# Optimization experiments

Measured on AMD Instinct MI355X. Metric: run time of the kernel, lower is better.

The kernel has to match this reference:

```python
import jax, jax.numpy as jnp
import numpy as np
from jax import lax

N_FFT = 512
HOP = 128
Q = N_FFT // HOP  # 4
KW = 2 * N_FFT - 1  # conv kernel width 1023


def _hann_periodic(n: int) -> np.ndarray:
    # scipy.signal.get_window('hann', n) default fftbins=True -> periodic hann
    k = np.arange(n)
    return (0.5 - 0.5 * np.cos(2.0 * np.pi * k / n)).astype(np.float64)


def _compute_alpha(W: np.ndarray, S: np.ndarray) -> np.ndarray:
    # Faithful port of ConsistencyLoss._compute_alpha (paper eq. 9)
    N, R = N_FFT, HOP
    alpha = np.zeros((2 * Q - 1, 2 * N - 1), dtype=np.complex64)
    for qi, q in enumerate(range(-(Q - 1), Q)):
        S_sh = np.zeros(N)
        s0, s1 = max(0, -q * R), min(N, N - q * R)
        if s0 < s1:
            S_sh[s0:s1] = S[q * R + s0: q * R + s1]
        term = W * S_sh
        f = np.fft.fft(term, 2 * N - 1)
        alpha[qi] = np.fft.fftshift(f) / N
    alpha[Q - 1, N - 1] -= 1.0
    return alpha


def setup_inputs() -> dict:
    key = jax.random.key(0)
    waveform = 0.1 * jax.random.normal(key, (4, 131072), dtype=jnp.float32)
    W_np = _hann_periodic(N_FFT)
    alpha = _compute_alpha(W_np, W_np)
    return {
        "waveform": waveform,
        "window": jnp.asarray(W_np, dtype=jnp.float32),
        "alpha_real": jnp.asarray(alpha.real, dtype=jnp.float32),
        "alpha_imag": jnp.asarray(alpha.imag, dtype=jnp.float32),
    }


def _stft(waveform, window):
    # torch.stft(center=True, pad_mode='reflect', onesided=True), output (B, T, F)
    N, hop = N_FFT, HOP
    B, L = waveform.shape
    padded = jnp.pad(waveform, ((0, 0), (N // 2, N // 2)), mode="reflect")
    T = 1 + L // hop
    idx = hop * jnp.arange(T)[:, None] + jnp.arange(N)[None, :]  # (T, N)
    frames = padded[:, idx] * window  # (B, T, N)
    return jnp.fft.rfft(frames, axis=-1)  # (B, T, N//2+1) complex64


def reference(waveform, window, alpha_real, alpha_imag):
    N, hop = N_FFT, HOP
    B = waveform.shape[0]
    H = _stft(waveform, window)  # (B, T, N//2+1)
    T = H.shape[1]

    # reconstruct full two-sided spectrum: concat conj-flipped interior bins
    H_full = jnp.concatenate([H, jnp.conj(H[:, :, 1:-1][:, :, ::-1])], axis=2)  # (B, T, N)
    H_full = jnp.transpose(H_full, (0, 2, 1))  # (B, N, T)

    # fuse the phase-term einsum into the per-frequency conv kernel:
    # C[b,n,t] = sum_q phase[n,q] * (alpha[q] * H_full[b,n])(t)
    #          = (K_eff[n] * H_full[b,n])(t),  K_eff = phase @ alpha
    q_idx = jnp.arange(-(Q - 1), Q, dtype=jnp.float32)
    n_idx = jnp.arange(N, dtype=jnp.float32)
    phase = jnp.exp(1j * (2.0 * jnp.pi / N) * n_idx[:, None] * q_idx[None, :])  # (N, 2Q-1)
    alpha = alpha_real + 1j * alpha_imag  # (2Q-1, KW)
    K = phase @ alpha.astype(jnp.complex64)  # (N, KW)
    Kr, Ki = jnp.real(K), jnp.imag(K)

    # complex depthwise (groups=N) cross-correlation via real 2-channel trick
    Hri = jnp.stack([jnp.real(H_full), jnp.imag(H_full)], axis=2).reshape(B, 2 * N, T)
    kern = jnp.stack([
        jnp.stack([Kr, -Ki], axis=1),  # real output rows (N, 2, KW)
        jnp.stack([Ki, Kr], axis=1),   # imag output rows (N, 2, KW)
    ], axis=1).reshape(2 * N, 2, KW)
    out = lax.conv_general_dilated(
        Hri, kern, window_strides=(1,), padding=[(N - 1, N - 1)],
        dimension_numbers=("NCH", "OIH", "NCH"), feature_group_count=N,
    )  # (B, 2N, T)
    Cr, Ci = out[:, 0::2], out[:, 1::2]  # (B, N, T)

    loss = jnp.sum(Cr * Cr + Ci * Ci)
    return loss / (B * T)
```

## Files before the change

### kernel.cpp

```cpp
#include <hip/hip_runtime.h>
#include <math.h>

#define T_FRAMES 1025
#define TSTRIDE  1032
#define BATCH    4
#define LWAV     131072
#define KWC      1023
#define MFFT     2048
#define PI_F     3.14159265358979323846f

struct c32 { float r, i; };
__device__ __forceinline__ c32 mkc(float r, float i){ c32 z; z.r=r; z.i=i; return z; }
__device__ __forceinline__ c32 cadd(c32 a, c32 b){ return mkc(a.r+b.r, a.i+b.i); }
__device__ __forceinline__ c32 csub(c32 a, c32 b){ return mkc(a.r-b.r, a.i-b.i); }
__device__ __forceinline__ c32 cmul(c32 a, c32 b){ return mkc(a.r*b.r - a.i*b.i, a.r*b.i + a.i*b.r); }
__device__ __forceinline__ c32 cni(c32 a){ return mkc(a.i, -a.r); }
#define C8F 0.70710678118654752440f
__device__ __forceinline__ c32 c8p(c32 a){ return mkc(C8F*(a.r+a.i), C8F*(a.i-a.r)); }
__device__ __forceinline__ c32 c8m(c32 a){ return mkc(C8F*(a.i-a.r), -C8F*(a.r+a.i)); }

__device__ __forceinline__ void st2(float2* X, int p, c32 v){ X[p] = make_float2(v.r, v.i); }
__device__ __forceinline__ c32 ld2(const float2* X, int p){ float2 e = X[p]; return mkc(e.x, e.y); }

__device__ __forceinline__ int pX(int j){ return j + (j >> 5); }
__device__ __forceinline__ int pS2(int j){ return j + (j >> 4); }
__device__ __forceinline__ int rev9(int j){ return (int)(__brev((unsigned)j) >> 23); }

__device__ __forceinline__ c32 wexp(int r) {
    float s, c;
    __sincosf((float)r * (-PI_F / 1024.0f), &s, &c);
    return mkc(c, s);
}

__device__ __forceinline__ void dif8_tw(c32 y[8], c32 w3) {
    c32 w2 = cmul(w3, w3), w1 = cmul(w2, w2);
    c32 u[8], v[8], d;
    d = csub(y[0], y[4]); u[0] = cadd(y[0], y[4]); u[4] = cmul(d, w3);
    d = csub(y[1], y[5]); u[1] = cadd(y[1], y[5]); u[5] = c8p(cmul(d, w3));
    d = csub(y[2], y[6]); u[2] = cadd(y[2], y[6]); u[6] = cni(cmul(d, w3));
    d = csub(y[3], y[7]); u[3] = cadd(y[3], y[7]); u[7] = c8m(cmul(d, w3));
    d = csub(u[0], u[2]); v[0] = cadd(u[0], u[2]); v[2] = cmul(d, w2);
    d = csub(u[1], u[3]); v[1] = cadd(u[1], u[3]); v[3] = cni(cmul(d, w2));
    d = csub(u[4], u[6]); v[4] = cadd(u[4], u[6]); v[6] = cmul(d, w2);
    d = csub(u[5], u[7]); v[5] = cadd(u[5], u[7]); v[7] = cni(cmul(d, w2));
    d = csub(v[0], v[1]); y[0] = cadd(v[0], v[1]); y[1] = cmul(d, w1);
    d = csub(v[2], v[3]); y[2] = cadd(v[2], v[3]); y[3] = cmul(d, w1);
    d = csub(v[4], v[5]); y[4] = cadd(v[4], v[5]); y[5] = cmul(d, w1);
    d = csub(v[6], v[7]); y[6] = cadd(v[6], v[7]); y[7] = cmul(d, w1);
}
__device__ __forceinline__ void dif8_nt(c32 y[8]) {
    c32 u[8], v[8], d;
    d = csub(y[0], y[4]); u[0] = cadd(y[0], y[4]); u[4] = d;
    d = csub(y[1], y[5]); u[1] = cadd(y[1], y[5]); u[5] = c8p(d);
    d = csub(y[2], y[6]); u[2] = cadd(y[2], y[6]); u[6] = cni(d);
    d = csub(y[3], y[7]); u[3] = cadd(y[3], y[7]); u[7] = c8m(d);
    d = csub(u[0], u[2]); v[0] = cadd(u[0], u[2]); v[2] = d;
    d = csub(u[1], u[3]); v[1] = cadd(u[1], u[3]); v[3] = cni(d);
    d = csub(u[4], u[6]); v[4] = cadd(u[4], u[6]); v[6] = d;
    d = csub(u[5], u[7]); v[5] = cadd(u[5], u[7]); v[7] = cni(d);
    d = csub(v[0], v[1]); y[0] = cadd(v[0], v[1]); y[1] = d;
    d = csub(v[2], v[3]); y[2] = cadd(v[2], v[3]); y[3] = d;
    d = csub(v[4], v[5]); y[4] = cadd(v[4], v[5]); y[5] = d;
    d = csub(v[6], v[7]); y[6] = cadd(v[6], v[7]); y[7] = d;
}
__device__ __forceinline__ void dit8_tw(c32 y[8], c32 w3) {
    c32 w2 = cmul(w3, w3), w1 = cmul(w2, w2);
    c32 u[8], v[8], t;
    t = cmul(y[1], w1); u[0] = cadd(y[0], t); u[1] = csub(y[0], t);
    t = cmul(y[3], w1); u[2] = cadd(y[2], t); u[3] = csub(y[2], t);
    t = cmul(y[5], w1); u[4] = cadd(y[4], t); u[5] = csub(y[4], t);
    t = cmul(y[7], w1); u[6] = cadd(y[6], t); u[7] = csub(y[6], t);
    t = cmul(u[2], w2);      v[0] = cadd(u[0], t); v[2] = csub(u[0], t);
    t = cni(cmul(u[3], w2)); v[1] = cadd(u[1], t); v[3] = csub(u[1], t);
    t = cmul(u[6], w2);      v[4] = cadd(u[4], t); v[6] = csub(u[4], t);
    t = cni(cmul(u[7], w2)); v[5] = cadd(u[5], t); v[7] = csub(u[5], t);
    t = cmul(v[4], w3);      y[0] = cadd(v[0], t); y[4] = csub(v[0], t);
    t = c8p(cmul(v[5], w3)); y[1] = cadd(v[1], t); y[5] = csub(v[1], t);
    t = cni(cmul(v[6], w3)); y[2] = cadd(v[2], t); y[6] = csub(v[2], t);
    t = c8m(cmul(v[7], w3)); y[3] = cadd(v[3], t); y[7] = csub(v[3], t);
}
__device__ __forceinline__ void dit8_nt(c32 y[8]) {
    c32 u[8], v[8], t;
    u[0] = cadd(y[0], y[1]); u[1] = csub(y[0], y[1]);
    u[2] = cadd(y[2], y[3]); u[3] = csub(y[2], y[3]);
    u[4] = cadd(y[4], y[5]); u[5] = csub(y[4], y[5]);
    u[6] = cadd(y[6], y[7]); u[7] = csub(y[6], y[7]);
    t = u[2];      v[0] = cadd(u[0], t); v[2] = csub(u[0], t);
    t = cni(u[3]); v[1] = cadd(u[1], t); v[3] = csub(u[1], t);
    t = u[6];      v[4] = cadd(u[4], t); v[6] = csub(u[4], t);
    t = cni(u[7]); v[5] = cadd(u[5], t); v[7] = csub(u[5], t);
    t = v[4];      y[0] = cadd(v[0], t); y[4] = csub(v[0], t);
    t = c8p(v[5]); y[1] = cadd(v[1], t); y[5] = csub(v[1], t);
    t = cni(v[6]); y[2] = cadd(v[2], t); y[6] = csub(v[2], t);
    t = c8m(v[7]); y[3] = cadd(v[3], t); y[7] = csub(v[3], t);
}
__device__ __forceinline__ void dif4(c32 y[4]) {
    c32 u0 = cadd(y[0], y[2]), d0 = csub(y[0], y[2]);
    c32 u1 = cadd(y[1], y[3]), d1 = cni(csub(y[1], y[3]));
    y[0] = cadd(u0, u1); y[1] = csub(u0, u1);
    y[2] = cadd(d0, d1); y[3] = csub(d0, d1);
}
__device__ __forceinline__ void dit4(c32 y[4], c32 w) {
    c32 w2 = cmul(w, w);
    c32 t1 = cmul(y[1], w2); c32 u0 = cadd(y[0], t1), u1 = csub(y[0], t1);
    c32 t3 = cmul(y[3], w2); c32 u2 = cadd(y[2], t3), u3 = csub(y[2], t3);
    c32 s2 = cmul(u2, w);      y[0] = cadd(u0, s2); y[2] = csub(u0, s2);
    c32 s3 = cni(cmul(u3, w)); y[1] = cadd(u1, s3); y[3] = csub(u1, s3);
}

__global__ __launch_bounds__(256) void stage1_kernel(const float* __restrict__ wave,
                                                     const float* __restrict__ win,
                                                     const float* __restrict__ ar,
                                                     const float* __restrict__ ai,
                                                     float2* __restrict__ Ht,
                                                     float2* __restrict__ Afbr,
                                                     float* __restrict__ out) {
    __shared__ float2 S2[4352];
    const int tid = threadIdx.x;

    if (blockIdx.x < 516) {
        float2* F = S2;
        const int w = tid >> 6, l = tid & 63;
        const int b = blockIdx.x / 129;
        const int t0 = (blockIdx.x - b * 129) << 3;
        const float* wb = wave + (size_t)b * LWAV;

        for (int pass = 0; pass < 2; ++pass) {
            const int j = w + (pass << 2);
            const int t = t0 + j;
            if (t < T_FRAMES) {
                c32 y[8];
#pragma unroll
                for (int k = 0; k < 8; ++k) {
                    int s = l + (k << 6);
                    int posn = t * 128 + s - 256;
                    int ix = posn < 0 ? -posn : (posn >= LWAV ? 2 * LWAV - 2 - posn : posn);
                    y[k] = mkc(wb[ix] * win[s], 0.f);
                }
                dif8_tw(y, wexp(l << 2));
#pragma unroll
                for (int k = 0; k < 8; ++k) st2(F, j*544 + pS2(l + (k << 6)), y[k]);
                __builtin_amdgcn_wave_barrier();
                {
                    int base = ((l >> 3) << 6) + (l & 7);
#pragma unroll
                    for (int k = 0; k < 8; ++k) y[k] = ld2(F, j*544 + pS2(base + (k << 3)));
                    dif8_tw(y, wexp((l & 7) << 5));
#pragma unroll
                    for (int k = 0; k < 8; ++k) st2(F, j*544 + pS2(base + (k << 3)), y[k]);
                }
                __builtin_amdgcn_wave_barrier();
                {
#pragma unroll
                    for (int k = 0; k < 8; ++k) y[k] = ld2(F, j*544 + pS2((l << 3) + k));
                    dif8_nt(y);
#pragma unroll
                    for (int k = 0; k < 8; ++k) st2(F, j*544 + pS2((l << 3) + k), y[k]);
                }
            }
        }
        __syncthreads();
        const bool full = (t0 + 7 < T_FRAMES);
#pragma unroll
        for (int h = 0; h < 2; ++h) {
            int p = tid + (h << 8);
            int bin = rev9(p);
            if (bin > 256) continue;
            int ps = pS2(p);
            size_t rowbase = (size_t)(b * 512 + p) * TSTRIDE + t0;
            if (full) {
                float4* dst = (float4*)(Ht + rowbase);
#pragma unroll
                for (int jj = 0; jj < 4; ++jj) {
                    float2 e0 = F[(2*jj)*544 + ps], e1 = F[(2*jj+1)*544 + ps];
                    dst[jj] = make_float4(e0.x, e0.y, e1.x, e1.y);
                }
            } else {
                for (int jj = 0; jj < 8; ++jj)
                    if (t0 + jj < T_FRAMES) Ht[rowbase + jj] = F[jj*544 + ps];
            }
        }
    } else if (blockIdx.x < 523) {
        float2* X = S2;
        const int q = blockIdx.x - 516;
        c32 y[8];
#pragma unroll
        for (int k = 0; k < 8; ++k) {
            int j = tid + (k << 8);
            y[k] = (j < KWC) ? mkc(ar[q * KWC + j], -ai[q * KWC + j]) : mkc(0.f, 0.f);
        }
        dif8_tw(y, wexp(tid));
#pragma unroll
        for (int k = 0; k < 8; ++k) st2(X, pX(tid + (k << 8)), y[k]);
        __syncthreads();
        {
            int base = ((tid >> 5) << 8) + (tid & 31);
#pragma unroll
            for (int k = 0; k < 8; ++k) y[k] = ld2(X, pX(base + (k << 5)));
            dif8_tw(y, wexp((tid & 31) << 3));
#pragma unroll
            for (int k = 0; k < 8; ++k) st2(X, pX(base + (k << 5)), y[k]);
        }
        __syncthreads();
        {
            int base = ((tid & 63) << 5) + (tid >> 6);
#pragma unroll
            for (int k = 0; k < 8; ++k) y[k] = ld2(X, pX(base + (k << 2)));
            dif8_tw(y, wexp((tid >> 6) << 6));
#pragma unroll
            for (int k = 0; k < 8; ++k) st2(X, pX(base + (k << 2)), y[k]);
        }
        __syncthreads();
#pragma unroll
        for (int h = 0; h < 2; ++h) {
            int g = tid + (h << 8);
            c32 z4[4];
#pragma unroll
            for (int k = 0; k < 4; ++k) z4[k] = ld2(X, pX((g << 2) + k));
            dif4(z4);
#pragma unroll
            for (int k = 0; k < 4; ++k) Afbr[(q << 11) + (g << 2) + k] = make_float2(z4[k].r, -z4[k].i);
        }
    } else {
        if (tid == 0) *out = 0.f;
    }
}

__global__ __launch_bounds__(256) void conv_kernel(const float2* __restrict__ Ht,
                                                   const float2* __restrict__ Afbr,
                                                   float* __restrict__ out) {
    __shared__ float2 S2[4224];
    __shared__ float red[4];
    float2* X0 = S2;
    float2* X1 = S2 + 2112;
    const int tid = threadIdx.x;
    const int g = blockIdx.x;
    const int half = g / 257;
    const int n = g - half * 257;
    const int b0 = half << 1;
    const int pr = rev9(n);

    const float2* row0 = Ht + (size_t)(b0 * 512 + pr) * TSTRIDE;
    const float2* row1 = Ht + (size_t)((b0 + 1) * 512 + pr) * TSTRIDE;

    c32 y0[8], y1[8];
#pragma unroll
    for (int k = 0; k < 8; ++k) {
        int j = tid + (k << 8);
        c32 v0 = mkc(0.f, 0.f), v1 = mkc(0.f, 0.f);
        if (j < T_FRAMES) {
            float2 h0 = row0[j]; v0 = mkc(h0.x, h0.y);
            float2 h1 = row1[j]; v1 = mkc(h1.x, h1.y);
        }
        y0[k] = v0; y1[k] = v1;
    }
    {
        c32 w3 = wexp(tid);
        dif8_tw(y0, w3);
        dif8_tw(y1, w3);
#pragma unroll
        for (int k = 0; k < 8; ++k) {
            int p = pX(tid + (k << 8));
            st2(X0, p, y0[k]); st2(X1, p, y1[k]);
        }
    }
    __syncthreads();
    {
        int base = ((tid >> 5) << 8) + (tid & 31);
#pragma unroll
        for (int k = 0; k < 8; ++k) {
            int p = pX(base + (k << 5));
            y0[k] = ld2(X0, p); y1[k] = ld2(X1, p);
        }
        c32 w3 = wexp((tid & 31) << 3);
        dif8_tw(y0, w3);
        dif8_tw(y1, w3);
#pragma unroll
        for (int k = 0; k < 8; ++k) {
            int p = pX(base + (k << 5));
            st2(X0, p, y0[k]); st2(X1, p, y1[k]);
        }
    }
    __syncthreads();
    {
        int base = ((tid & 63) << 5) + (tid >> 6);
#pragma unroll
        for (int k = 0; k < 8; ++k) {
            int p = pX(base + (k << 2));
            y0[k] = ld2(X0, p); y1[k] = ld2(X1, p);
        }
        c32 w3 = wexp((tid >> 6) << 6);
        dif8_tw(y0, w3);
        dif8_tw(y1, w3);
#pragma unroll
        for (int k = 0; k < 8; ++k) {
            int p = pX(base + (k << 2));
            st2(X0, p, y0[k]); st2(X1, p, y1[k]);
        }
    }
    __syncthreads();
    {
        c32 p1 = wexp(-(n << 2));
        c32 p2 = cmul(p1, p1);
        c32 p3 = cmul(p2, p1);
        const int a0 = tid << 3;
        const int p0 = pX(a0);
#pragma unroll
        for (int k = 0; k < 8; ++k) {
            y0[k] = ld2(X0, p0 + k);
            y1[k] = ld2(X1, p0 + k);
        }
        dif4(&y0[0]); dif4(&y0[4]);
        dif4(&y1[0]); dif4(&y1[4]);
        const float4* af4 = (const float4*)(Afbr + a0);
#pragma unroll
        for (int k = 0; k < 8; ++k) {
            float4 a;
            c32 Kk;
            a = af4[(3 << 10) + (k >> 1)];
            float ax = (k & 1) ? a.z : a.x, ay = (k & 1) ? a.w : a.y;
            Kk = mkc(ax, ay);
            a = af4[(4 << 10) + (k >> 1)]; ax = (k & 1) ? a.z : a.x; ay = (k & 1) ? a.w : a.y;
            Kk.r += p1.r * ax - p1.i * ay;  Kk.i += p1.r * ay + p1.i * ax;
            a = af4[(2 << 10) + (k >> 1)]; ax = (k & 1) ? a.z : a.x; ay = (k & 1) ? a.w : a.y;
            Kk.r += p1.r * ax + p1.i * ay;  Kk.i += p1.r * ay - p1.i * ax;
            a = af4[(5 << 10) + (k >> 1)]; ax = (k & 1) ? a.z : a.x; ay = (k & 1) ? a.w : a.y;
            Kk.r += p2.r * ax - p2.i * ay;  Kk.i += p2.r * ay + p2.i * ax;
            a = af4[(1 << 10) + (k >> 1)]; ax = (k & 1) ? a.z : a.x; ay = (k & 1) ? a.w : a.y;
            Kk.r += p2.r * ax + p2.i * ay;  Kk.i += p2.r * ay - p2.i * ax;
            a = af4[(6 << 10) + (k >> 1)]; ax = (k & 1) ? a.z : a.x; ay = (k & 1) ? a.w : a.y;
            Kk.r += p3.r * ax - p3.i * ay;  Kk.i += p3.r * ay + p3.i * ax;
            a = af4[(0 << 10) + (k >> 1)]; ax = (k & 1) ? a.z : a.x; ay = (k & 1) ? a.w : a.y;
            Kk.r += p3.r * ax + p3.i * ay;  Kk.i += p3.r * ay - p3.i * ax;
            c32 P0 = cmul(y0[k], Kk);
            c32 P1 = cmul(y1[k], Kk);
            y0[k] = mkc(P0.r, -P0.i);
            y1[k] = mkc(P1.r, -P1.i);
        }
        dit8_nt(y0);
        dit8_nt(y1);
#pragma unroll
        for (int k = 0; k < 8; ++k) {
            st2(X0, p0 + k, y0[k]);
            st2(X1, p0 + k, y1[k]);
        }
    }
    __syncthreads();
    {
        int G = (((tid & 63) >> 3) << 2) + (tid >> 6);
        int pos = tid & 7;
        int base = (G << 6) + pos;
#pragma unroll
        for (int k = 0; k < 8; ++k) {
            int p = pX(base + (k << 3));
            y0[k] = ld2(X0, p); y1[k] = ld2(X1, p);
        }
        c32 w3 = wexp(pos << 5);
        dit8_tw(y0, w3);
        dit8_tw(y1, w3);
#pragma unroll
        for (int k = 0; k < 8; ++k) {
            int p = pX(base + (k << 3));
            st2(X0, p, y0[k]); st2(X1, p, y1[k]);
        }
    }
    __syncthreads();
    {
        int base = ((tid >> 6) << 9) + (tid & 63);
#pragma unroll
        for (int k = 0; k < 8; ++k) {
            int p = pX(base + (k << 6));
            y0[k] = ld2(X0, p); y1[k] = ld2(X1, p);
        }
        c32 w3 = wexp((tid & 63) << 2);
        dit8_tw(y0, w3);
        dit8_tw(y1, w3);
#pragma unroll
        for (int k = 0; k < 8; ++k) {
            int p = pX(base + (k << 6));
            st2(X0, p, y0[k]); st2(X1, p, y1[k]);
        }
    }
    __syncthreads();
    float local = 0.f;
#pragma unroll
    for (int h = 0; h < 2; ++h) {
        int pos = tid + (h << 8);
        c32 w = wexp(pos);
        c32 z0[4], z1[4];
#pragma unroll
        for (int k = 0; k < 4; ++k) {
            int p = pX(pos + (k << 9));
            z0[k] = ld2(X0, p); z1[k] = ld2(X1, p);
        }
        dit4(z0, w);
        dit4(z1, w);
        local += z0[0].r * z0[0].r + z0[0].i * z0[0].i
               + z1[0].r * z1[0].r + z1[0].i * z1[0].i;
        if (pos < 2)  local += z0[1].r * z0[1].r + z0[1].i * z0[1].i
                             + z1[1].r * z1[1].r + z1[1].i * z1[1].i;
        if (pos >= 1) local += z0[3].r * z0[3].r + z0[3].i * z0[3].i
                             + z1[3].r * z1[3].r + z1[3].i * z1[3].i;
    }
    local *= (n == 0 || n == 256) ? 1.0f : 2.0f;
#pragma unroll
    for (int off = 32; off >= 1; off >>= 1) local += __shfl_down(local, off);
    if ((tid & 63) == 0) red[tid >> 6] = local;
    __syncthreads();
    if (tid == 0) {
        const float SCALE =
            (float)(1.0 / ((double)MFFT * (double)MFFT * (double)BATCH * (double)T_FRAMES));
        atomicAdd(out, (red[0] + red[1] + red[2] + red[3]) * SCALE);
    }
}

extern "C" void kernel_launch(void* const* d_in, const int* in_sizes, int n_in,
                              void* d_out, int out_size, void* d_ws, size_t ws_size,
                              hipStream_t stream) {
    (void)in_sizes; (void)n_in; (void)out_size; (void)ws_size;
    const float* wave   = (const float*)d_in[0];
    const float* window = (const float*)d_in[1];
    const float* ar     = (const float*)d_in[2];
    const float* ai     = (const float*)d_in[3];
    float* out = (float*)d_out;

    char* ws = (char*)d_ws;
    float2* Ht   = (float2*)ws;
    float2* Afbr = (float2*)(ws + 16908288);

    stage1_kernel<<<524, 256, 0, stream>>>(wave, window, ar, ai, Ht, Afbr, out);
    conv_kernel<<<2 * 257, 256, 0, stream>>>(Ht, Afbr, out);
}
```

Baseline: 87.52 us.

## Restructure conv FFT stages to wave-local passes and exploit sparse input/output

The 2048-point FFT in the conv kernel is reordered so the middle stages run on 512-point chunks owned by one wavefront, replacing several block-wide __syncthreads with wave barriers. The first pass uses the fact that only 1025 input samples are nonzero, and the last pass computes only the output rows that feed the loss. The stage-1 Ht write is also reorganized into coalesced per-frame stores with a padded LDS stride. This adds indexing complexity and carries a risk of subtle stage-order or twiddle errors.

```diff
diff --git a/kernel.cpp b/kernel.cpp
--- a/kernel.cpp
+++ b/kernel.cpp
@@ -100,6 +100,15 @@
     y[0] = cadd(u0, u1); y[1] = csub(u0, u1);
     y[2] = cadd(d0, d1); y[3] = csub(d0, d1);
 }
+__device__ __forceinline__ void dif4_tw(c32 y[4], c32 w) {
+    c32 w2 = cmul(w, w), w3 = cmul(w2, w);
+    c32 s0 = cadd(y[0], y[2]), d0 = csub(y[0], y[2]);
+    c32 s1 = cadd(y[1], y[3]), d1 = cni(csub(y[1], y[3]));
+    y[0] = cadd(s0, s1);
+    y[1] = cmul(csub(s0, s1), w2);
+    y[2] = cmul(cadd(d0, d1), w);
+    y[3] = cmul(csub(d0, d1), w3);
+}
 __device__ __forceinline__ void dit4(c32 y[4], c32 w) {
     c32 w2 = cmul(w, w);
     c32 t1 = cmul(y[1], w2); c32 u0 = cadd(y[0], t1), u1 = csub(y[0], t1);
@@ -108,6 +117,7 @@
     c32 s3 = cni(cmul(u3, w)); y[1] = cadd(u1, s3); y[3] = csub(u1, s3);
 }
 
+#define FSTR 546
 __global__ __launch_bounds__(256) void stage1_kernel(const float* __restrict__ wave,
                                                      const float* __restrict__ win,
                                                      const float* __restrict__ ar,
@@ -115,7 +125,7 @@
                                                      float2* __restrict__ Ht,
                                                      float2* __restrict__ Afbr,
                                                      float* __restrict__ out) {
-    __shared__ float2 S2[4352];
+    __shared__ float2 S2[4368];
     const int tid = threadIdx.x;
 
     if (blockIdx.x < 516) {
@@ -139,46 +149,38 @@
                 }
                 dif8_tw(y, wexp(l << 2));
 #pragma unroll
-                for (int k = 0; k < 8; ++k) st2(F, j*544 + pS2(l + (k << 6)), y[k]);
+                for (int k = 0; k < 8; ++k) st2(F, j*FSTR + pS2(l + (k << 6)), y[k]);
                 __builtin_amdgcn_wave_barrier();
                 {
                     int base = ((l >> 3) << 6) + (l & 7);
 #pragma unroll
-                    for (int k = 0; k < 8; ++k) y[k] = ld2(F, j*544 + pS2(base + (k << 3)));
+                    for (int k = 0; k < 8; ++k) y[k] = ld2(F, j*FSTR + pS2(base + (k << 3)));
                     dif8_tw(y, wexp((l & 7) << 5));
 #pragma unroll
-                    for (int k = 0; k < 8; ++k) st2(F, j*544 + pS2(base + (k << 3)), y[k]);
+                    for (int k = 0; k < 8; ++k) st2(F, j*FSTR + pS2(base + (k << 3)), y[k]);
                 }
                 __builtin_amdgcn_wave_barrier();
                 {
 #pragma unroll
-                    for (int k = 0; k < 8; ++k) y[k] = ld2(F, j*544 + pS2((l << 3) + k));
+                    for (int k = 0; k < 8; ++k) y[k] = ld2(F, j*FSTR + pS2((l << 3) + k));
                     dif8_nt(y);
 #pragma unroll
-                    for (int k = 0; k < 8; ++k) st2(F, j*544 + pS2((l << 3) + k), y[k]);
+                    for (int k = 0; k < 8; ++k) st2(F, j*FSTR + pS2((l << 3) + k), y[k]);
                 }
             }
         }
         __syncthreads();
-        const bool full = (t0 + 7 < T_FRAMES);
-#pragma unroll
-        for (int h = 0; h < 2; ++h) {
-            int p = tid + (h << 8);
-            int bin = rev9(p);
-            if (bin > 256) continue;
-            int ps = pS2(p);
-            size_t rowbase = (size_t)(b * 512 + p) * TSTRIDE + t0;
-            if (full) {
-                float4* dst = (float4*)(Ht + rowbase);
-#pragma unroll
-                for (int jj = 0; jj < 4; ++jj) {
-                    float2 e0 = F[(2*jj)*544 + ps], e1 = F[(2*jj+1)*544 + ps];
-                    dst[jj] = make_float4(e0.x, e0.y, e1.x, e1.y);
-                }
-            } else {
-                for (int jj = 0; jj < 8; ++jj)
-                    if (t0 + jj < T_FRAMES) Ht[rowbase + jj] = F[jj*544 + ps];
+        const int jj = tid & 7;
+        const int rb = tid >> 3;
+        const bool tok = (t0 + jj < T_FRAMES);
+        if (tok) {
+#pragma unroll
+            for (int rr = 0; rr < 8; ++rr) {
+                int p = ((rr << 5) + rb) << 1;
+                Ht[(size_t)(b * 512 + p) * TSTRIDE + t0 + jj] = F[jj*FSTR + pS2(p)];
             }
+            if (tid < 8)
+                Ht[(size_t)(b * 512 + 1) * TSTRIDE + t0 + jj] = F[jj*FSTR + pS2(1)];
         }
     } else if (blockIdx.x < 523) {
         float2* X = S2;
@@ -234,6 +236,7 @@
     float2* X0 = S2;
     float2* X1 = S2 + 2112;
     const int tid = threadIdx.x;
+    const int l = tid & 63, wv = tid >> 6;
     const int g = blockIdx.x;
     const int half = g / 257;
     const int n = g - half * 257;
@@ -243,165 +246,163 @@
     const float2* row0 = Ht + (size_t)(b0 * 512 + pr) * TSTRIDE;
     const float2* row1 = Ht + (size_t)((b0 + 1) * 512 + pr) * TSTRIDE;
 
+    const c32 wA  = wexp(tid);
+    const c32 wB  = wexp((l & 31) << 3);
+    const c32 wP3 = wexp((l & 7) << 5);
+    const c32 wI2 = wexp((l & 3) << 6);
+
     c32 y0[8], y1[8];
 #pragma unroll
+    for (int k = 0; k < 4; ++k) {
+        float2 h0 = row0[tid + (k << 8)]; y0[k] = mkc(h0.x, h0.y);
+        float2 h1 = row1[tid + (k << 8)]; y1[k] = mkc(h1.x, h1.y);
+    }
+    if (tid == 0) {
+        float2 h0 = row0[1024]; y0[4] = mkc(h0.x, h0.y);
+        float2 h1 = row1[1024]; y1[4] = mkc(h1.x, h1.y);
+    } else { y0[4] = mkc(0.f, 0.f); y1[4] = mkc(0.f, 0.f); }
+#pragma unroll
+    for (int k = 5; k < 8; ++k) { y0[k] = mkc(0.f, 0.f); y1[k] = mkc(0.f, 0.f); }
+    dif8_tw(y0, wA);
+    dif8_tw(y1, wA);
+#pragma unroll
     for (int k = 0; k < 8; ++k) {
-        int j = tid + (k << 8);
-        c32 v0 = mkc(0.f, 0.f), v1 = mkc(0.f, 0.f);
-        if (j < T_FRAMES) {
-            float2 h0 = row0[j]; v0 = mkc(h0.x, h0.y);
-            float2 h1 = row1[j]; v1 = mkc(h1.x, h1.y);
-        }
-        y0[k] = v0; y1[k] = v1;
-    }
+        int p = pX(tid + (k << 8));
+        st2(X0, p, y0[k]); st2(X1, p, y1[k]);
+    }
+    __syncthreads();
+
+    const int Bb = (((wv << 1) + (l >> 5)) << 8) + (l & 31);
+#pragma unroll
+    for (int gg = 0; gg < 2; ++gg)
+#pragma unroll
+        for (int t = 0; t < 4; ++t) {
+            int p = pX(Bb + (gg << 5) + (t << 6));
+            y0[gg*4+t] = ld2(X0, p); y1[gg*4+t] = ld2(X1, p);
+        }
     {
-        c32 w3 = wexp(tid);
-        dif8_tw(y0, w3);
-        dif8_tw(y1, w3);
-#pragma unroll
-        for (int k = 0; k < 8; ++k) {
-            int p = pX(tid + (k << 8));
-            st2(X0, p, y0[k]); st2(X1, p, y1[k]);
-        }
-    }
-    __syncthreads();
-    {
-        int base = ((tid >> 5) << 8) + (tid & 31);
-#pragma unroll
-        for (int k = 0; k < 8; ++k) {
-            int p = pX(base + (k << 5));
-            y0[k] = ld2(X0, p); y1[k] = ld2(X1, p);
-        }
-        c32 w3 = wexp((tid & 31) << 3);
-        dif8_tw(y0, w3);
-        dif8_tw(y1, w3);
-#pragma unroll
-        for (int k = 0; k < 8; ++k) {
-            int p = pX(base + (k << 5));
-            st2(X0, p, y0[k]); st2(X1, p, y1[k]);
-        }
-    }
-    __syncthreads();
-    {
-        int base = ((tid & 63) << 5) + (tid >> 6);
-#pragma unroll
-        for (int k = 0; k < 8; ++k) {
-            int p = pX(base + (k << 2));
-            y0[k] = ld2(X0, p); y1[k] = ld2(X1, p);
-        }
-        c32 w3 = wexp((tid >> 6) << 6);
-        dif8_tw(y0, w3);
-        dif8_tw(y1, w3);
-#pragma unroll
-        for (int k = 0; k < 8; ++k) {
-            int p = pX(base + (k << 2));
-            st2(X0, p, y0[k]); st2(X1, p, y1[k]);
-        }
-    }
-    __syncthreads();
+        c32 wg1 = c8p(wB);
+        dif4_tw(&y0[0], wB); dif4_tw(&y0[4], wg1);
+        dif4_tw(&y1[0], wB); dif4_tw(&y1[4], wg1);
+    }
+#pragma unroll
+    for (int gg = 0; gg < 2; ++gg)
+#pragma unroll
+        for (int t = 0; t < 4; ++t) {
+            int p = pX(Bb + (gg << 5) + (t << 6));
+            st2(X0, p, y0[gg*4+t]); st2(X1, p, y1[gg*4+t]);
+        }
+    __builtin_amdgcn_wave_barrier();
+
+    const int chunk = wv << 9;
+    const int p3b = chunk + ((l >> 3) << 6) + (l & 7);
+#pragma unroll
+    for (int u = 0; u < 8; ++u) {
+        int p = pX(p3b + (u << 3));
+        y0[u] = ld2(X0, p); y1[u] = ld2(X1, p);
+    }
+    dif8_tw(y0, wP3);
+    dif8_tw(y1, wP3);
+#pragma unroll
+    for (int u = 0; u < 8; ++u) {
+        int p = pX(p3b + (u << 3));
+        st2(X0, p, y0[u]); st2(X1, p, y1[u]);
+    }
+    __builtin_amdgcn_wave_barrier();
+
+    const int pos0 = chunk + ((l >> 3) << 6) + ((l & 7) << 3);
+    const int px0 = pX(pos0);
+#pragma unroll
+    for (int u = 0; u < 8; ++u) { y0[u] = ld2(X0, px0 + u); y1[u] = ld2(X1, px0 + u); }
+    dif8_nt(y0);
+    dif8_nt(y1);
     {
         c32 p1 = wexp(-(n << 2));
         c32 p2 = cmul(p1, p1);
         c32 p3 = cmul(p2, p1);
-        const int a0 = tid << 3;
-        const int p0 = pX(a0);
-#pragma unroll
-        for (int k = 0; k < 8; ++k) {
-            y0[k] = ld2(X0, p0 + k);
-            y1[k] = ld2(X1, p0 + k);
-        }
-        dif4(&y0[0]); dif4(&y0[4]);
-        dif4(&y1[0]); dif4(&y1[4]);
-        const float4* af4 = (const float4*)(Afbr + a0);
+        const float4* af4 = (const float4*)Afbr;
+        const int afb = pos0 >> 1;
 #pragma unroll
         for (int k = 0; k < 8; ++k) {
             float4 a;
             c32 Kk;
-            a = af4[(3 << 10) + (k >> 1)];
+            a = af4[(3 << 10) + afb + (k >> 1)];
             float ax = (k & 1) ? a.z : a.x, ay = (k & 1) ? a.w : a.y;
             Kk = mkc(ax, ay);
-            a = af4[(4 << 10) + (k >> 1)]; ax = (k & 1) ? a.z : a.x; ay = (k & 1) ? a.w : a.y;
+            a = af4[(4 << 10) + afb + (k >> 1)]; ax = (k & 1) ? a.z : a.x; ay = (k & 1) ? a.w : a.y;
             Kk.r += p1.r * ax - p1.i * ay;  Kk.i += p1.r * ay + p1.i * ax;
-            a = af4[(2 << 10) + (k >> 1)]; ax = (k & 1) ? a.z : a.x; ay = (k & 1) ? a.w : a.y;
+            a = af4[(2 << 10) + afb + (k >> 1)]; ax = (k & 1) ? a.z : a.x; ay = (k & 1) ? a.w : a.y;
             Kk.r += p1.r * ax + p1.i * ay;  Kk.i += p1.r * ay - p1.i * ax;
-            a = af4[(5 << 10) + (k >> 1)]; ax = (k & 1) ? a.z : a.x; ay = (k & 1) ? a.w : a.y;
+            a = af4[(5 << 10) + afb + (k >> 1)]; ax = (k & 1) ? a.z : a.x; ay = (k & 1) ? a.w : a.y;
             Kk.r += p2.r * ax - p2.i * ay;  Kk.i += p2.r * ay + p2.i * ax;
-            a = af4[(1 << 10) + (k >> 1)]; ax = (k & 1) ? a.z : a.x; ay = (k & 1) ? a.w : a.y;
+            a = af4[(1 << 10) + afb + (k >> 1)]; ax = (k & 1) ? a.z : a.x; ay = (k & 1) ? a.w : a.y;
             Kk.r += p2.r * ax + p2.i * ay;  Kk.i += p2.r * ay - p2.i * ax;
-            a = af4[(6 << 10) + (k >> 1)]; ax = (k & 1) ? a.z : a.x; ay = (k & 1) ? a.w : a.y;
+            a = af4[(6 << 10) + afb + (k >> 1)]; ax = (k & 1) ? a.z : a.x; ay = (k & 1) ? a.w : a.y;
             Kk.r += p3.r * ax - p3.i * ay;  Kk.i += p3.r * ay + p3.i * ax;
-            a = af4[(0 << 10) + (k >> 1)]; ax = (k & 1) ? a.z : a.x; ay = (k & 1) ? a.w : a.y;
+            a = af4[(0 << 10) + afb + (k >> 1)]; ax = (k & 1) ? a.z : a.x; ay = (k & 1) ? a.w : a.y;
             Kk.r += p3.r * ax + p3.i * ay;  Kk.i += p3.r * ay - p3.i * ax;
             c32 P0 = cmul(y0[k], Kk);
             c32 P1 = cmul(y1[k], Kk);
             y0[k] = mkc(P0.r, -P0.i);
             y1[k] = mkc(P1.r, -P1.i);
         }
-        dit8_nt(y0);
-        dit8_nt(y1);
-#pragma unroll
-        for (int k = 0; k < 8; ++k) {
-            st2(X0, p0 + k, y0[k]);
-            st2(X1, p0 + k, y1[k]);
-        }
+    }
+    dit8_nt(y0);
+    dit8_nt(y1);
+#pragma unroll
+    for (int u = 0; u < 8; ++u) { st2(X0, px0 + u, y0[u]); st2(X1, px0 + u, y1[u]); }
+    __builtin_amdgcn_wave_barrier();
+
+    const int i2b = chunk + ((l >> 2) << 5) + (l & 3);
+#pragma unroll
+    for (int gg = 0; gg < 2; ++gg)
+#pragma unroll
+        for (int t = 0; t < 4; ++t) {
+            int p = pX(i2b + (gg << 2) + (t << 3));
+            y0[gg*4+t] = ld2(X0, p); y1[gg*4+t] = ld2(X1, p);
+        }
+    {
+        c32 wg1 = c8p(wI2);
+        dit4(&y0[0], wI2); dit4(&y0[4], wg1);
+        dit4(&y1[0], wI2); dit4(&y1[4], wg1);
+    }
+#pragma unroll
+    for (int gg = 0; gg < 2; ++gg)
+#pragma unroll
+        for (int t = 0; t < 4; ++t) {
+            int p = pX(i2b + (gg << 2) + (t << 3));
+            st2(X0, p, y0[gg*4+t]); st2(X1, p, y1[gg*4+t]);
+        }
+    __builtin_amdgcn_wave_barrier();
+
+    const int i3b = chunk + ((l >> 5) << 8) + (l & 31);
+#pragma unroll
+    for (int k = 0; k < 8; ++k) {
+        int p = pX(i3b + (k << 5));
+        y0[k] = ld2(X0, p); y1[k] = ld2(X1, p);
+    }
+    dit8_tw(y0, wB);
+    dit8_tw(y1, wB);
+#pragma unroll
+    for (int k = 0; k < 8; ++k) {
+        int p = pX(i3b + (k << 5));
+        st2(X0, p, y0[k]); st2(X1, p, y1[k]);
     }
     __syncthreads();
-    {
-        int G = (((tid & 63) >> 3) << 2) + (tid >> 6);
-        int pos = tid & 7;
-        int base = (G << 6) + pos;
-#pragma unroll
-        for (int k = 0; k < 8; ++k) {
-            int p = pX(base + (k << 3));
-            y0[k] = ld2(X0, p); y1[k] = ld2(X1, p);
-        }
-        c32 w3 = wexp(pos << 5);
-        dit8_tw(y0, w3);
-        dit8_tw(y1, w3);
-#pragma unroll
-        for (int k = 0; k < 8; ++k) {
-            int p = pX(base + (k << 3));
-            st2(X0, p, y0[k]); st2(X1, p, y1[k]);
-        }
-    }
-    __syncthreads();
-    {
-        int base = ((tid >> 6) << 9) + (tid & 63);
-#pragma unroll
-        for (int k = 0; k < 8; ++k) {
-            int p = pX(base + (k << 6));
-            y0[k] = ld2(X0, p); y1[k] = ld2(X1, p);
-        }
-        c32 w3 = wexp((tid & 63) << 2);
-        dit8_tw(y0, w3);
-        dit8_tw(y1, w3);
-#pragma unroll
-        for (int k = 0; k < 8; ++k) {
-            int p = pX(base + (k << 6));
-            st2(X0, p, y0[k]); st2(X1, p, y1[k]);
-        }
-    }
-    __syncthreads();
-    float local = 0.f;
-#pragma unroll
-    for (int h = 0; h < 2; ++h) {
-        int pos = tid + (h << 8);
-        c32 w = wexp(pos);
-        c32 z0[4], z1[4];
-#pragma unroll
-        for (int k = 0; k < 4; ++k) {
-            int p = pX(pos + (k << 9));
-            z0[k] = ld2(X0, p); z1[k] = ld2(X1, p);
-        }
-        dit4(z0, w);
-        dit4(z1, w);
-        local += z0[0].r * z0[0].r + z0[0].i * z0[0].i
-               + z1[0].r * z1[0].r + z1[0].i * z1[0].i;
-        if (pos < 2)  local += z0[1].r * z0[1].r + z0[1].i * z0[1].i
-                             + z1[1].r * z1[1].r + z1[1].i * z1[1].i;
-        if (pos >= 1) local += z0[3].r * z0[3].r + z0[3].i * z0[3].i
-                             + z1[3].r * z1[3].r + z1[3].i * z1[3].i;
-    }
+
+#pragma unroll
+    for (int k = 0; k < 8; ++k) {
+        int p = pX(tid + (k << 8));
+        y0[k] = ld2(X0, p); y1[k] = ld2(X1, p);
+    }
+    dit8_tw(y0, wA);
+    dit8_tw(y1, wA);
+    float local = y0[0].r*y0[0].r + y0[0].i*y0[0].i + y1[0].r*y1[0].r + y1[0].i*y1[0].i
+                + y0[1].r*y0[1].r + y0[1].i*y0[1].i + y1[1].r*y1[1].r + y1[1].i*y1[1].i
+                + y0[7].r*y0[7].r + y0[7].i*y0[7].i + y1[7].r*y1[7].r + y1[7].i*y1[7].i;
+    if (tid < 2)  local += y0[2].r*y0[2].r + y0[2].i*y0[2].i + y1[2].r*y1[2].r + y1[2].i*y1[2].i;
+    if (tid >= 1) local += y0[6].r*y0[6].r + y0[6].i*y0[6].i + y1[6].r*y1[6].r + y1[6].i*y1[6].i;
+
     local *= (n == 0 || n == 256) ? 1.0f : 2.0f;
 #pragma unroll
     for (int off = 32; off >= 1; off >>= 1) local += __shfl_down(local, off);
```

Result: faster. 84.46 us (-3.5%).
